# Kernel tuning notes

Hardware: AMD Instinct MI355X
Metric: run time of the kernel (lower is better)

## Reference

```python
import jax, jax.numpy as jnp
import numpy as np


def setup_inputs() -> dict:
    key = jax.random.key(0)
    k1, k2, k3 = jax.random.split(key, 3)
    B, C, H, W = 32, 2048, 14, 14
    OUT = 512
    x = jax.random.normal(k1, (B, C, H, W), dtype=jnp.float32)
    gamma = jnp.zeros((1,), dtype=jnp.float32)  # nn.Parameter(torch.zeros(1))
    # 1x1 conv 2048 -> 512 (layer=4 branch), kaiming-ish scale
    conv_w = jax.random.normal(k2, (OUT, C, 1, 1), dtype=jnp.float32) * (1.0 / np.sqrt(C))
    conv_b = jax.random.normal(k3, (OUT,), dtype=jnp.float32) * 0.01
    return {"x": x, "gamma": gamma, "conv_w": conv_w, "conv_b": conv_b}


def reference(x, gamma, conv_w, conv_b):
    B, C, H, W = x.shape
    q = x.reshape(B, C, H * W)                      # [B, C, N]
    # energy[b, c, d] = <q[b,c,:], q[b,d,:]>
    energy = jnp.einsum('bcn,bdn->bcd', q, q)       # [B, C, C]
    # max-subtract trick: softmax(max - energy) along last dim
    energy_new = jnp.max(energy, axis=-1, keepdims=True) - energy
    attention = jax.nn.softmax(energy_new, axis=-1)  # [B, C, C]
    out = jnp.einsum('bcd,bdn->bcn', attention, q).reshape(B, C, H, W)
    out = gamma * out + x
    # 1x1 conv, stride 1, no padding (layer=4 branch)
    pam_out = jax.lax.conv_general_dilated(
        out, conv_w, window_strides=(1, 1), padding='VALID',
        dimension_numbers=('NCHW', 'OIHW', 'NCHW'))
    pam_out = pam_out + conv_b[None, :, None, None]
    return pam_out
```

## Files before the change

### kernel.cpp

```cpp
#include <hip/hip_runtime.h>
#include <hip/hip_bf16.h>
#include <stdint.h>

#define B_   32
#define C_   2048
#define HW_  196
#define OUT_ 512
#define KT_  64
#define MT_  64
#define BP16 136

typedef short short8 __attribute__((ext_vector_type(8)));
typedef float floatx4 __attribute__((ext_vector_type(4)));
typedef unsigned short u16;

__device__ __forceinline__ u16 f2bf(float f) {
  union { float f; uint32_t u; } v; v.f = f;
  return (u16)((v.u + 0x8000u) >> 16);
}

__device__ __forceinline__ uint32_t pack_bf16(float a, float b) {
  union { __hip_bfloat162 h; uint32_t u; } c;
  c.h = __float22bfloat162_rn(make_float2(a, b));
  return c.u;
}

__global__ void wcvt_kernel(const float* __restrict__ w, u16* __restrict__ wbf) {
  int gid = blockIdx.x * 256 + threadIdx.x;
  float4 v = ((const float4*)w)[gid];
  ((uint2*)wbf)[gid] = make_uint2(pack_bf16(v.x, v.y), pack_bf16(v.z, v.w));
}

__global__ void attn_fallback(const float* __restrict__ x, const float* __restrict__ gamma,
                              float* __restrict__ y) {
  float g = gamma[0];
  if (g == 0.0f) return;
  __shared__ float qc[HW_];
  __shared__ float e[C_];
  __shared__ float red[256];
  int tid = threadIdx.x;
  for (int cRow = blockIdx.x; cRow < C_; cRow += gridDim.x) {
    for (int b = 0; b < B_; ++b) {
      const float* q = x + (size_t)b * C_ * HW_;
      __syncthreads();
      for (int i = tid; i < HW_; i += 256) qc[i] = q[(size_t)cRow * HW_ + i];
      __syncthreads();
      for (int d = tid; d < C_; d += 256) {
        float s = 0.f;
        const float* qd = q + (size_t)d * HW_;
        for (int n = 0; n < HW_; ++n) s += qc[n] * qd[n];
        e[d] = s;
      }
      __syncthreads();
      float mn = 3.4e38f;
      for (int d = tid; d < C_; d += 256) mn = fminf(mn, e[d]);
      red[tid] = mn; __syncthreads();
      for (int s = 128; s > 0; s >>= 1) { if (tid < s) red[tid] = fminf(red[tid], red[tid + s]); __syncthreads(); }
      float emin = red[0];
      __syncthreads();
      float ps = 0.f;
      for (int d = tid; d < C_; d += 256) { float p = __expf(emin - e[d]); e[d] = p; ps += p; }
      red[tid] = ps; __syncthreads();
      for (int s = 128; s > 0; s >>= 1) { if (tid < s) red[tid] += red[tid + s]; __syncthreads(); }
      float S = red[0];
      __syncthreads();
      float invS = 1.f / S;
      for (int n = tid; n < HW_; n += 256) {
        float acc = 0.f;
        for (int d = 0; d < C_; ++d) acc += e[d] * q[(size_t)d * HW_ + n];
        y[((size_t)b * C_ + cRow) * HW_ + n] = g * acc * invS + q[(size_t)cRow * HW_ + n];
      }
    }
  }
}

__global__ __launch_bounds__(256, 2) void conv_gemm(
    const float* __restrict__ x, const float* __restrict__ yws,
    const u16* __restrict__ wbf, const float* __restrict__ bias,
    const float* __restrict__ gamma, float* __restrict__ out) {

  __shared__ __align__(16) u16 Bs[112 * BP16];

  const float* src = (gamma[0] != 0.f) ? yws : x;

  int bid = blockIdx.x;
  int xcd = bid & 7;
  int s   = bid >> 3;
  int ot  = s & 7;
  int g   = ((s >> 3) << 3) | xcd;
  int b   = g >> 1;
  int nh  = g & 1;
  int oBase = ot * MT_;
  int n0    = nh * 112;
  int nLim  = HW_ - n0;
  if (nLim > 112) nLim = 112;

  int tid  = threadIdx.x;
  int wave = tid >> 6;
  int lane = tid & 63;
  int col  = lane & 15;
  int quad = lane >> 4;

  const float* xb = src + (size_t)b * C_ * HW_;
  int oWave = oBase + wave * 16 + col;

  floatx4 acc[7];
#pragma unroll
  for (int i = 0; i < 7; ++i) { floatx4 z = {0.f, 0.f, 0.f, 0.f}; acc[i] = z; }

  int sN[7], sCq[7]; bool sV[7];
#pragma unroll
  for (int i = 0; i < 7; ++i) {
    int slot = i * 256 + tid;
    sN[i]  = slot % 112;
    sCq[i] = slot / 112;
    sV[i]  = (n0 + sN[i]) < HW_;
  }

  float4 bReg[7];
  uint4  aReg[2], aRegN[2];

  auto loadB = [&](int kBase) {
#pragma unroll
    for (int i = 0; i < 7; ++i) {
      if (sV[i]) {
        const float* p = xb + (size_t)(kBase + sCq[i] * 4) * HW_ + n0 + sN[i];
        bReg[i].x = p[0];
        bReg[i].y = p[HW_];
        bReg[i].z = p[2 * HW_];
        bReg[i].w = p[3 * HW_];
      }
    }
  };
  auto loadA = [&](uint4* dst, int kBase) {
#pragma unroll
    for (int ks = 0; ks < 2; ++ks)
      dst[ks] = *(const uint4*)(wbf + (size_t)oWave * C_ + kBase + ks * 32 + quad * 8);
  };

  loadB(0);
  loadA(aReg, 0);

  for (int kt = 0; kt < C_ / KT_; ++kt) {
    __syncthreads();
#pragma unroll
    for (int i = 0; i < 7; ++i) {
      uint32_t d0 = pack_bf16(bReg[i].x, bReg[i].y);
      uint32_t d1 = pack_bf16(bReg[i].z, bReg[i].w);
      *(uint2*)&Bs[sN[i] * BP16 + sCq[i] * 4] = make_uint2(d0, d1);
    }
    __syncthreads();

    if (kt + 1 < C_ / KT_) {
      loadB((kt + 1) * KT_);
      loadA(aRegN, (kt + 1) * KT_);
    }

#pragma unroll
    for (int ks = 0; ks < 2; ++ks) {
      union { uint4 u; short8 v; } af; af.u = aReg[ks];
#pragma unroll
      for (int nt = 0; nt < 7; ++nt) {
        short8 bf = *(const short8*)&Bs[(nt * 16 + col) * BP16 + ks * 32 + quad * 8];
        acc[nt] = __builtin_amdgcn_mfma_f32_16x16x32_bf16(af.v, bf, acc[nt], 0, 0, 0);
      }
    }
    aReg[0] = aRegN[0]; aReg[1] = aRegN[1];
  }

  float* outb = out + (size_t)b * OUT_ * HW_;
#pragma unroll
  for (int r = 0; r < 4; ++r) {
    int o = oBase + wave * 16 + quad * 4 + r;
    float bv = bias[o];
    float* orow = outb + (size_t)o * HW_ + n0;
#pragma unroll
    for (int nt = 0; nt < 7; ++nt) {
      int nl = nt * 16 + col;
      if (nl < nLim) orow[nl] = acc[nt][r] + bv;
    }
  }
}

extern "C" void kernel_launch(void* const* d_in, const int* in_sizes, int n_in,
                              void* d_out, int out_size, void* d_ws, size_t ws_size,
                              hipStream_t stream) {
  const float* x      = (const float*)d_in[0];
  const float* gamma  = (const float*)d_in[1];
  const float* conv_w = (const float*)d_in[2];
  const float* conv_b = (const float*)d_in[3];
  float* out = (float*)d_out;

  const size_t wbf_bytes = (size_t)OUT_ * C_ * sizeof(u16);
  const size_t y_bytes   = (size_t)B_ * C_ * HW_ * sizeof(float);
  u16*   wbf = (u16*)d_ws;
  float* yws = (float*)((char*)d_ws + wbf_bytes);
  bool have_fallback_ws = ws_size >= wbf_bytes + y_bytes;
  const float* ysrc = have_fallback_ws ? (const float*)yws : x;

  wcvt_kernel<<<dim3((OUT_ * C_) / 4 / 256), dim3(256), 0, stream>>>(conv_w, wbf);
  if (have_fallback_ws)
    attn_fallback<<<dim3(256), dim3(256), 0, stream>>>(x, gamma, yws);
  conv_gemm<<<dim3(512), dim3(256), 0, stream>>>(x, ysrc, wbf, conv_b, gamma, out);
}
```

Measured before the change: 144.7 us.

## Stage conv input via async global-to-LDS loads and skip padded N tiles

Replaces the per-thread strided scalar loads of the activation tile, which were held in registers, with 16-byte global_load_lds transfers into an fp32 LDS staging buffer. A separate pass then converts the staged data to bf16 in the padded B layout. The second N half now runs only 6 MFMA column tiles instead of 7. In exchange, LDS use per block roughly doubles. The MFMA and epilogue loops now take a runtime trip count and index the accumulator array, which may push the accumulators to scratch memory.

```diff
diff --git a/kernel.cpp b/kernel.cpp
--- a/kernel.cpp
+++ b/kernel.cpp
@@ -14,15 +14,16 @@
 typedef float floatx4 __attribute__((ext_vector_type(4)));
 typedef unsigned short u16;
 
-__device__ __forceinline__ u16 f2bf(float f) {
-  union { float f; uint32_t u; } v; v.f = f;
-  return (u16)((v.u + 0x8000u) >> 16);
-}
-
 __device__ __forceinline__ uint32_t pack_bf16(float a, float b) {
   union { __hip_bfloat162 h; uint32_t u; } c;
   c.h = __float22bfloat162_rn(make_float2(a, b));
   return c.u;
+}
+
+__device__ __forceinline__ void async_ld16(const float* g, void* lds_base) {
+  __builtin_amdgcn_global_load_lds(
+      (const __attribute__((address_space(1))) uint32_t*)g,
+      (__attribute__((address_space(3))) uint32_t*)lds_base, 16, 0, 0);
 }
 
 __global__ void wcvt_kernel(const float* __restrict__ w, u16* __restrict__ wbf) {
@@ -79,7 +80,8 @@
     const u16* __restrict__ wbf, const float* __restrict__ bias,
     const float* __restrict__ gamma, float* __restrict__ out) {
 
-  __shared__ __align__(16) u16 Bs[112 * BP16];
+  __shared__ __align__(16) u16   Bs[112 * BP16];
+  __shared__ __align__(16) float stageF[64 * 112];
 
   const float* src = (gamma[0] != 0.f) ? yws : x;
 
@@ -92,8 +94,9 @@
   int nh  = g & 1;
   int oBase = ot * MT_;
   int n0    = nh * 112;
-  int nLim  = HW_ - n0;
-  if (nLim > 112) nLim = 112;
+  int nF    = nh ? 84 : 112;
+  int nCh   = nF >> 2;
+  int nTi   = nh ? 6 : 7;
 
   int tid  = threadIdx.x;
   int wave = tid >> 6;
@@ -108,59 +111,64 @@
 #pragma unroll
   for (int i = 0; i < 7; ++i) { floatx4 z = {0.f, 0.f, 0.f, 0.f}; acc[i] = z; }
 
-  int sN[7], sCq[7]; bool sV[7];
-#pragma unroll
-  for (int i = 0; i < 7; ++i) {
-    int slot = i * 256 + tid;
-    sN[i]  = slot % 112;
-    sCq[i] = slot / 112;
-    sV[i]  = (n0 + sN[i]) < HW_;
-  }
-
-  float4 bReg[7];
-  uint4  aReg[2], aRegN[2];
-
-  auto loadB = [&](int kBase) {
-#pragma unroll
-    for (int i = 0; i < 7; ++i) {
-      if (sV[i]) {
-        const float* p = xb + (size_t)(kBase + sCq[i] * 4) * HW_ + n0 + sN[i];
-        bReg[i].x = p[0];
-        bReg[i].y = p[HW_];
-        bReg[i].z = p[2 * HW_];
-        bReg[i].w = p[3 * HW_];
-      }
-    }
+  const float* gJ[7];  bool jV[7];  int jIdx[7];
+  for (int jj = 0; jj < 7; ++jj) {
+    int j = wave + 4 * jj;
+    jV[jj]   = j < nCh;
+    jIdx[jj] = j;
+    int s16  = j * 64 + lane;
+    int c    = s16 / nCh;
+    int ch   = s16 - c * nCh;
+    gJ[jj] = xb + (size_t)c * HW_ + n0 + ch * 4;
+  }
+  int cN[7], cCg[7]; bool cV[7];
+  for (int v = 0; v < 7; ++v) {
+    int u  = v * 256 + tid;
+    cV[v]  = u < 16 * nF;
+    int cg = u / nF;
+    cN[v]  = u - cg * nF;
+    cCg[v] = cg;
+  }
+
+  auto issueStage = [&](int kBase) {
+#pragma unroll
+    for (int jj = 0; jj < 7; ++jj)
+      if (jV[jj])
+        async_ld16(gJ[jj] + (size_t)kBase * HW_, (char*)stageF + jIdx[jj] * 1024);
   };
+
+  uint4 aReg[2], aRegN[2];
   auto loadA = [&](uint4* dst, int kBase) {
 #pragma unroll
     for (int ks = 0; ks < 2; ++ks)
       dst[ks] = *(const uint4*)(wbf + (size_t)oWave * C_ + kBase + ks * 32 + quad * 8);
   };
 
-  loadB(0);
+  issueStage(0);
   loadA(aReg, 0);
 
   for (int kt = 0; kt < C_ / KT_; ++kt) {
     __syncthreads();
 #pragma unroll
-    for (int i = 0; i < 7; ++i) {
-      uint32_t d0 = pack_bf16(bReg[i].x, bReg[i].y);
-      uint32_t d1 = pack_bf16(bReg[i].z, bReg[i].w);
-      *(uint2*)&Bs[sN[i] * BP16 + sCq[i] * 4] = make_uint2(d0, d1);
+    for (int v = 0; v < 7; ++v) {
+      if (cV[v]) {
+        const float* sp = &stageF[cCg[v] * 4 * nF + cN[v]];
+        float f0 = sp[0], f1 = sp[nF], f2 = sp[2 * nF], f3 = sp[3 * nF];
+        *(uint2*)&Bs[cN[v] * BP16 + cCg[v] * 4] =
+            make_uint2(pack_bf16(f0, f1), pack_bf16(f2, f3));
+      }
     }
     __syncthreads();
 
     if (kt + 1 < C_ / KT_) {
-      loadB((kt + 1) * KT_);
+      issueStage((kt + 1) * KT_);
       loadA(aRegN, (kt + 1) * KT_);
     }
 
 #pragma unroll
     for (int ks = 0; ks < 2; ++ks) {
       union { uint4 u; short8 v; } af; af.u = aReg[ks];
-#pragma unroll
-      for (int nt = 0; nt < 7; ++nt) {
+      for (int nt = 0; nt < nTi; ++nt) {
         short8 bf = *(const short8*)&Bs[(nt * 16 + col) * BP16 + ks * 32 + quad * 8];
         acc[nt] = __builtin_amdgcn_mfma_f32_16x16x32_bf16(af.v, bf, acc[nt], 0, 0, 0);
       }
@@ -168,14 +176,14 @@
     aReg[0] = aRegN[0]; aReg[1] = aRegN[1];
   }
 
+  int nLim = HW_ - n0; if (nLim > 112) nLim = 112;
   float* outb = out + (size_t)b * OUT_ * HW_;
 #pragma unroll
   for (int r = 0; r < 4; ++r) {
     int o = oBase + wave * 16 + quad * 4 + r;
     float bv = bias[o];
     float* orow = outb + (size_t)o * HW_ + n0;
-#pragma unroll
-    for (int nt = 0; nt < 7; ++nt) {
+    for (int nt = 0; nt < nTi; ++nt) {
       int nl = nt * 16 + col;
       if (nl < nLim) orow[nl] = acc[nt][r] + bv;
     }
```

Measured after the change: 165.3 us. +14.3%, slower.

## Pre-transpose activations to swizzled bf16 tiles and async-load GEMM operands into LDS

Applied to the files above, without the earlier changes.

A new kernel converts the conv input to bf16 and transposes it into XOR-swizzled 64-channel tiles. The weight conversion kernel writes weights in a matching swizzled tile layout. The 1x1-conv GEMM then streams both operands straight into double-buffered LDS with global_load_lds and vmcnt waits, instead of doing strided fp32 loads, register conversion and LDS stores. This is meant to cut the GEMM's load latency and per-iteration conversion work. In exchange it adds an extra kernel launch and a full round trip of a padded bf16 copy of the activations through memory.

```diff
diff --git a/kernel.cpp b/kernel.cpp
--- a/kernel.cpp
+++ b/kernel.cpp
@@ -7,17 +7,14 @@
 #define HW_  196
 #define OUT_ 512
 #define KT_  64
+#define NKT  32
 #define MT_  64
-#define BP16 136
 
 typedef short short8 __attribute__((ext_vector_type(8)));
 typedef float floatx4 __attribute__((ext_vector_type(4)));
 typedef unsigned short u16;
 
-__device__ __forceinline__ u16 f2bf(float f) {
-  union { float f; uint32_t u; } v; v.f = f;
-  return (u16)((v.u + 0x8000u) >> 16);
-}
+#define VMCNT_WAIT(n) __builtin_amdgcn_s_waitcnt(0x0F70 | (n))
 
 __device__ __forceinline__ uint32_t pack_bf16(float a, float b) {
   union { __hip_bfloat162 h; uint32_t u; } c;
@@ -25,10 +22,26 @@
   return c.u;
 }
 
-__global__ void wcvt_kernel(const float* __restrict__ w, u16* __restrict__ wbf) {
-  int gid = blockIdx.x * 256 + threadIdx.x;
-  float4 v = ((const float4*)w)[gid];
-  ((uint2*)wbf)[gid] = make_uint2(pack_bf16(v.x, v.y), pack_bf16(v.z, v.w));
+__device__ __forceinline__ void async_ld16(const u16* g, void* lds_base) {
+  __builtin_amdgcn_global_load_lds(
+      (const __attribute__((address_space(1))) uint32_t*)g,
+      (__attribute__((address_space(3))) uint32_t*)lds_base, 16, 0, 0);
+}
+
+__global__ void wcvt_kernel(const float* __restrict__ w, u16* __restrict__ wa) {
+  int G  = blockIdx.x * 256 + threadIdx.x;
+  int o  = G >> 8;
+  int ck = G & 255;
+  int kt = ck >> 3, kc = ck & 7;
+  const float* s = w + (size_t)o * C_ + kt * KT_ + kc * 8;
+  float4 v0 = *(const float4*)s;
+  float4 v1 = *(const float4*)(s + 4);
+  uint4 c;
+  c.x = pack_bf16(v0.x, v0.y); c.y = pack_bf16(v0.z, v0.w);
+  c.z = pack_bf16(v1.x, v1.y); c.w = pack_bf16(v1.z, v1.w);
+  int TA    = (o >> 6) * NKT + kt;
+  int chunk = (o & 63) * 8 + (kc ^ (o & 7));
+  *(uint4*)(wa + (size_t)TA * 4096 + chunk * 8) = c;
 }
 
 __global__ void attn_fallback(const float* __restrict__ x, const float* __restrict__ gamma,
@@ -74,14 +87,52 @@
   }
 }
 
+__global__ __launch_bounds__(256) void xpose_kernel(
+    const float* __restrict__ x, const float* __restrict__ ysrc,
+    const float* __restrict__ gamma, u16* __restrict__ xt) {
+  __shared__ float tile[64 * 196];
+  const float* src = (gamma[0] != 0.f) ? ysrc : x;
+  int b  = blockIdx.x >> 5;
+  int kt = blockIdx.x & 31;
+  const float* sb = src + ((size_t)b * C_ + kt * KT_) * HW_;
+  int tid = threadIdx.x;
+  for (int r = 0; r < 13; ++r) {
+    int u = r * 256 + tid;
+    if (u < 3136) {
+      int ci = u / 49, n4 = u - ci * 49;
+      *(float4*)&tile[ci * 196 + n4 * 4] = *(const float4*)(sb + (size_t)ci * HW_ + n4 * 4);
+    }
+  }
+  __syncthreads();
+#pragma unroll
+  for (int nh = 0; nh < 2; ++nh) {
+    int valid = nh ? 84 : 112;
+    u16* dst = xt + ((size_t)(b * 2 + nh) * NKT + kt) * 8192;
+#pragma unroll
+    for (int i = 0; i < 4; ++i) {
+      int q   = i * 256 + tid;
+      int n   = q >> 3;
+      int pos = q & 7;
+      int kc  = pos ^ (n & 7);
+      uint4 val = make_uint4(0u, 0u, 0u, 0u);
+      if (n < valid) {
+        const float* tp = &tile[kc * 8 * 196 + nh * 112 + n];
+        val.x = pack_bf16(tp[0 * 196], tp[1 * 196]);
+        val.y = pack_bf16(tp[2 * 196], tp[3 * 196]);
+        val.z = pack_bf16(tp[4 * 196], tp[5 * 196]);
+        val.w = pack_bf16(tp[6 * 196], tp[7 * 196]);
+      }
+      *(uint4*)(dst + q * 8) = val;
+    }
+  }
+}
+
 __global__ __launch_bounds__(256, 2) void conv_gemm(
-    const float* __restrict__ x, const float* __restrict__ yws,
-    const u16* __restrict__ wbf, const float* __restrict__ bias,
-    const float* __restrict__ gamma, float* __restrict__ out) {
-
-  __shared__ __align__(16) u16 Bs[112 * BP16];
-
-  const float* src = (gamma[0] != 0.f) ? yws : x;
+    const u16* __restrict__ xt, const u16* __restrict__ wa,
+    const float* __restrict__ bias, float* __restrict__ out) {
+
+  __shared__ __align__(16) u16 Ab[2][4096];
+  __shared__ __align__(16) u16 Bb[2][8192];
 
   int bid = blockIdx.x;
   int xcd = bid & 7;
@@ -92,8 +143,7 @@
   int nh  = g & 1;
   int oBase = ot * MT_;
   int n0    = nh * 112;
-  int nLim  = HW_ - n0;
-  if (nLim > 112) nLim = 112;
+  int nLim  = nh ? 84 : 112;
 
   int tid  = threadIdx.x;
   int wave = tid >> 6;
@@ -101,72 +151,59 @@
   int col  = lane & 15;
   int quad = lane >> 4;
 
-  const float* xb = src + (size_t)b * C_ * HW_;
-  int oWave = oBase + wave * 16 + col;
+  const u16* Abase = wa + (size_t)(ot * NKT) * 4096 + lane * 8;
+  const u16* Bbase = xt + (size_t)((b * 2 + nh) * NKT) * 8192 + lane * 8;
 
   floatx4 acc[7];
 #pragma unroll
   for (int i = 0; i < 7; ++i) { floatx4 z = {0.f, 0.f, 0.f, 0.f}; acc[i] = z; }
 
-  int sN[7], sCq[7]; bool sV[7];
-#pragma unroll
-  for (int i = 0; i < 7; ++i) {
-    int slot = i * 256 + tid;
-    sN[i]  = slot % 112;
-    sCq[i] = slot / 112;
-    sV[i]  = (n0 + sN[i]) < HW_;
-  }
-
-  float4 bReg[7];
-  uint4  aReg[2], aRegN[2];
-
-  auto loadB = [&](int kBase) {
-#pragma unroll
-    for (int i = 0; i < 7; ++i) {
-      if (sV[i]) {
-        const float* p = xb + (size_t)(kBase + sCq[i] * 4) * HW_ + n0 + sN[i];
-        bReg[i].x = p[0];
-        bReg[i].y = p[HW_];
-        bReg[i].z = p[2 * HW_];
-        bReg[i].w = p[3 * HW_];
-      }
-    }
+  int aOffB = wave * 2048;
+  int bOffB = wave * 4096;
+
+  auto issue = [&](int sel, int kt) {
+    const u16* as = Abase + (size_t)kt * 4096 + wave * 1024;
+    const u16* bs = Bbase + (size_t)kt * 8192 + wave * 2048;
+    char* al = (char*)Ab[sel] + aOffB;
+    char* bl = (char*)Bb[sel] + bOffB;
+    async_ld16(as,        al);
+    async_ld16(as + 512,  al + 1024);
+#pragma unroll
+    for (int jj = 0; jj < 4; ++jj)
+      async_ld16(bs + jj * 512, bl + jj * 1024);
   };
-  auto loadA = [&](uint4* dst, int kBase) {
-#pragma unroll
-    for (int ks = 0; ks < 2; ++ks)
-      dst[ks] = *(const uint4*)(wbf + (size_t)oWave * C_ + kBase + ks * 32 + quad * 8);
+
+  auto phase = [&](int sel) {
+    const u16* A = Ab[sel];
+    const u16* Bq = Bb[sel];
+#pragma unroll
+    for (int ks = 0; ks < 2; ++ks) {
+      int cb = ks * 4 + quad;
+      int o  = wave * 16 + col;
+      union { short8 v; } af;
+      af.v = *(const short8*)&A[o * 64 + ((cb ^ (o & 7)) * 8)];
+#pragma unroll
+      for (int nt = 0; nt < 7; ++nt) {
+        int n = nt * 16 + col;
+        short8 bf = *(const short8*)&Bq[n * 64 + ((cb ^ (n & 7)) * 8)];
+        acc[nt] = __builtin_amdgcn_mfma_f32_16x16x32_bf16(af.v, bf, acc[nt], 0, 0, 0);
+      }
+    }
   };
 
-  loadB(0);
-  loadA(aReg, 0);
-
-  for (int kt = 0; kt < C_ / KT_; ++kt) {
-    __syncthreads();
-#pragma unroll
-    for (int i = 0; i < 7; ++i) {
-      uint32_t d0 = pack_bf16(bReg[i].x, bReg[i].y);
-      uint32_t d1 = pack_bf16(bReg[i].z, bReg[i].w);
-      *(uint2*)&Bs[sN[i] * BP16 + sCq[i] * 4] = make_uint2(d0, d1);
-    }
-    __syncthreads();
-
-    if (kt + 1 < C_ / KT_) {
-      loadB((kt + 1) * KT_);
-      loadA(aRegN, (kt + 1) * KT_);
-    }
-
-#pragma unroll
-    for (int ks = 0; ks < 2; ++ks) {
-      union { uint4 u; short8 v; } af; af.u = aReg[ks];
-#pragma unroll
-      for (int nt = 0; nt < 7; ++nt) {
-        short8 bf = *(const short8*)&Bs[(nt * 16 + col) * BP16 + ks * 32 + quad * 8];
-        acc[nt] = __builtin_amdgcn_mfma_f32_16x16x32_bf16(af.v, bf, acc[nt], 0, 0, 0);
-      }
-    }
-    aReg[0] = aRegN[0]; aReg[1] = aRegN[1];
-  }
+  issue(0, 0);
+  issue(1, 1);
+#pragma unroll 1
+  for (int kt = 0; kt < NKT - 1; ++kt) {
+    VMCNT_WAIT(6);
+    __builtin_amdgcn_s_barrier();
+    phase(kt & 1);
+    __builtin_amdgcn_s_barrier();
+    if (kt < NKT - 2) issue(kt & 1, kt + 2);
+  }
+  VMCNT_WAIT(0);
+  __builtin_amdgcn_s_barrier();
+  phase(1);
 
   float* outb = out + (size_t)b * OUT_ * HW_;
 #pragma unroll
@@ -191,15 +228,18 @@
   const float* conv_b = (const float*)d_in[3];
   float* out = (float*)d_out;
 
-  const size_t wbf_bytes = (size_t)OUT_ * C_ * sizeof(u16);
-  const size_t y_bytes   = (size_t)B_ * C_ * HW_ * sizeof(float);
-  u16*   wbf = (u16*)d_ws;
-  float* yws = (float*)((char*)d_ws + wbf_bytes);
-  bool have_fallback_ws = ws_size >= wbf_bytes + y_bytes;
+  const size_t wa_bytes = (size_t)OUT_ * C_ * sizeof(u16);
+  const size_t xt_bytes = (size_t)B_ * 2 * NKT * 8192 * sizeof(u16);
+  const size_t y_bytes  = (size_t)B_ * C_ * HW_ * sizeof(float);
+  u16*   wa  = (u16*)d_ws;
+  u16*   xt  = (u16*)((char*)d_ws + wa_bytes);
+  float* yws = (float*)((char*)d_ws + wa_bytes + xt_bytes);
+  bool have_fallback_ws = ws_size >= wa_bytes + xt_bytes + y_bytes;
   const float* ysrc = have_fallback_ws ? (const float*)yws : x;
 
-  wcvt_kernel<<<dim3((OUT_ * C_) / 4 / 256), dim3(256), 0, stream>>>(conv_w, wbf);
+  wcvt_kernel<<<dim3(512), dim3(256), 0, stream>>>(conv_w, wa);
   if (have_fallback_ws)
     attn_fallback<<<dim3(256), dim3(256), 0, stream>>>(x, gamma, yws);
-  conv_gemm<<<dim3(512), dim3(256), 0, stream>>>(x, ysrc, wbf, conv_b, gamma, out);
-}
+  xpose_kernel<<<dim3(B_ * NKT), dim3(256), 0, stream>>>(x, ysrc, gamma, xt);
+  conv_gemm<<<dim3(512), dim3(256), 0, stream>>>(xt, wa, conv_b, out);
+}
```

After: 133.8 us. 1.08x faster.
